# Kernel optimization log

Hardware: AMD Instinct MI355X
Metric: run time of the kernel (lower is better)

Reference implementation:

```python
import jax, jax.numpy as jnp
import numpy as np

B_, L_, STATE_DIM = 16, 1024, 17
D_MODEL, D_STATE, D_CONV, EXPAND, N_LAYERS = 512, 128, 4, 2, 6
HEADDIM = 64
D_INNER = EXPAND * D_MODEL              # 1024
NHEADS = D_INNER // HEADDIM             # 16
CONV_DIM = D_INNER + 2 * D_STATE        # 1280
D_IN_PROJ = 2 * D_INNER + 2 * D_STATE + NHEADS  # 2320


def _silu(x):
    return x * jax.nn.sigmoid(x)


def _layernorm(x, g, b, eps=1e-5):
    mu = jnp.mean(x, -1, keepdims=True)
    xc = x - mu
    var = jnp.mean(xc * xc, -1, keepdims=True)
    return xc * jax.lax.rsqrt(var + eps) * g + b


def _rope(x):
    # pairs are consecutive elements, matching x.view(B,L,d//2,2) in torch
    B, L, d = x.shape
    inv_freq = 1.0 / (10000.0 ** (jnp.arange(0, d, 2, dtype=jnp.float32) / d))
    freqs = jnp.arange(L, dtype=jnp.float32)[:, None] * inv_freq[None, :]  # [L, d/2]
    cos, sin = jnp.cos(freqs), jnp.sin(freqs)
    xr = x.reshape(B, L, d // 2, 2)
    x1, x2 = xr[..., 0], xr[..., 1]
    out = jnp.stack([x1 * cos - x2 * sin, x1 * sin + x2 * cos], axis=-1)
    return out.reshape(B, L, d)


def _causal_conv1d(x, w, b):
    # depthwise causal conv: x [B,L,C], w [C,K], b [C]
    K = w.shape[1]
    L = x.shape[1]
    xp = jnp.pad(x, ((0, 0), (K - 1, 0), (0, 0)))
    y = b
    for k in range(K):
        y = y + xp[:, k:k + L, :] * w[:, k]
    return y


def _mamba2(x, in_w, conv_w, conv_b, dt_bias, A_log, Dp, rms_w, out_w):
    # Mamba2 block (ngroups=1, headdim=64, gated RMSNorm, no proj biases)
    B, L, _ = x.shape
    zxbcdt = x @ in_w                              # [B,L,D_IN_PROJ]
    z = zxbcdt[..., :D_INNER]
    xBC = zxbcdt[..., D_INNER:D_INNER + CONV_DIM]
    dt = zxbcdt[..., D_INNER + CONV_DIM:]          # [B,L,H]
    xBC = _silu(_causal_conv1d(xBC, conv_w, conv_b))
    xs = xBC[..., :D_INNER].reshape(B, L, NHEADS, HEADDIM)
    Bm = xBC[..., D_INNER:D_INNER + D_STATE]       # [B,L,N]
    Cm = xBC[..., D_INNER + D_STATE:]              # [B,L,N]
    dt = jax.nn.softplus(dt + dt_bias)             # [B,L,H]
    A = -jnp.exp(A_log)                            # [H]
    decay = jnp.exp(dt * A)                        # [B,L,H]

    def step(h, inp):
        xt, Bt, Ct, dc, dtt = inp                  # [B,H,P],[B,N],[B,N],[B,H],[B,H]
        h = h * dc[..., None, None] + (dtt[..., None] * xt)[..., None] * Bt[:, None, None, :]
        yt = jnp.einsum('bhpn,bn->bhp', h, Ct)
        return h, yt

    h0 = jnp.zeros((B, NHEADS, HEADDIM, D_STATE), x.dtype)
    xs_t = jnp.moveaxis(xs, 1, 0)
    _, ys = jax.lax.scan(step, h0, (xs_t, jnp.moveaxis(Bm, 1, 0), jnp.moveaxis(Cm, 1, 0), jnp.moveaxis(decay, 1, 0), jnp.moveaxis(dt, 1, 0)))
    y = jnp.moveaxis(ys, 0, 1) + Dp[None, None, :, None] * xs  # [B,L,H,P]
    y = y.reshape(B, L, D_INNER)
    y = y * _silu(z)                               # gated
    y = y * jax.lax.rsqrt(jnp.mean(y * y, -1, keepdims=True) + 1e-5) * rms_w
    return y @ out_w


def setup_inputs():
    key = jax.random.key(0)
    ks = jax.random.split(key, 8)

    def rn(k, shape, scale):
        return jax.random.normal(k, shape, jnp.float32) * scale

    return dict(
        states=rn(ks[0], (B_, L_, STATE_DIM), 1.0),
        input_proj_w=rn(ks[1], (STATE_DIM, D_MODEL), STATE_DIM ** -0.5),
        input_proj_b=jnp.zeros((D_MODEL,), jnp.float32),
        ln_g=jnp.ones((N_LAYERS, D_MODEL), jnp.float32),
        ln_b=jnp.zeros((N_LAYERS, D_MODEL), jnp.float32),
        in_proj_w=rn(ks[2], (N_LAYERS, D_MODEL, D_IN_PROJ), D_MODEL ** -0.5),
        conv_w=rn(ks[3], (N_LAYERS, CONV_DIM, D_CONV), D_CONV ** -0.5),
        conv_b=jnp.zeros((N_LAYERS, CONV_DIM), jnp.float32),
        dt_bias=rn(ks[4], (N_LAYERS, NHEADS), 0.5) - 4.0,
        A_log=jnp.log(jax.random.uniform(ks[5], (N_LAYERS, NHEADS), jnp.float32, 1.0, 16.0)),
        D_param=jnp.ones((N_LAYERS, NHEADS), jnp.float32),
        rms_w=jnp.ones((N_LAYERS, D_INNER), jnp.float32),
        out_proj_w=rn(ks[6], (N_LAYERS, D_INNER, D_MODEL), D_INNER ** -0.5),
        post_ln_g=jnp.ones((D_MODEL,), jnp.float32),
        post_ln_b=jnp.zeros((D_MODEL,), jnp.float32),
        output_proj_w=rn(ks[7], (D_MODEL, D_MODEL), D_MODEL ** -0.5),
        output_proj_b=jnp.zeros((D_MODEL,), jnp.float32),
    )


def reference(states, input_proj_w, input_proj_b, ln_g, ln_b, in_proj_w, conv_w, conv_b,
              dt_bias, A_log, D_param, rms_w, out_proj_w, post_ln_g, post_ln_b,
              output_proj_w, output_proj_b):
    x = states @ input_proj_w + input_proj_b
    x = _rope(x)
    for l in range(N_LAYERS):
        h = _layernorm(x, ln_g[l], ln_b[l])
        h = _mamba2(h, in_proj_w[l], conv_w[l], conv_b[l], dt_bias[l], A_log[l],
                    D_param[l], rms_w[l], out_proj_w[l])
        x = x + h  # dropout is identity in eval mode
    x = _layernorm(x, post_ln_g, post_ln_b)
    return x @ output_proj_w + output_proj_b
```

## Files before the change

### kernel.cpp

```cpp
#include <hip/hip_runtime.h>
#include <hip/hip_bf16.h>
#include <cstdint>
#include <cstddef>


#define B_      16
#define L_      1024
#define NTOK    (B_ * L_)
#define DMODEL  512
#define DINNER  1024
#define NHEADS  16
#define HEADDIM 64
#define DSTATE  128
#define CONVDIM 1280
#define DINPROJ 2320
#define NPADT   2432
#define NLAYERS 6
#define LC      128
#define NC      8
#define SP      136
#define CCH     64
#define LOG2E   1.4426950408889634f

typedef short s8v  __attribute__((ext_vector_type(8)));
typedef float f4v  __attribute__((ext_vector_type(4)));
typedef unsigned short u8v __attribute__((ext_vector_type(8)));

__device__ __forceinline__ float b2f(unsigned short u) {
  unsigned v = ((unsigned)u) << 16;
  return __builtin_bit_cast(float, v);
}
__device__ __forceinline__ unsigned short f2b(float f) {
  unsigned u = __builtin_bit_cast(unsigned, f);
  u += 0x7fffu + ((u >> 16) & 1u);
  return (unsigned short)(u >> 16);
}
__device__ __forceinline__ void gl_lds16(const unsigned short* g, unsigned short* l) {
  __builtin_amdgcn_global_load_lds(
      (const __attribute__((address_space(1))) unsigned int*)g,
      (__attribute__((address_space(3))) unsigned int*)l, 16, 0, 0);
}

__global__ void k_flag(const unsigned int* __restrict__ lng_raw, int* __restrict__ flag) {
  *flag = (lng_raw[0] == 0x3F800000u) ? 0 : 1;
}

struct Cvt12 {
  const void* src[12];
  unsigned short* dst[12];
  int n[12];
};

__global__ __launch_bounds__(256) void k_convert_multi(
    Cvt12 jobs, const int* __restrict__ flag)
{
  const int f = *flag;
  const int e = blockIdx.y;
  const int n = jobs.n[e];
  const void* __restrict__ src = jobs.src[e];
  unsigned short* __restrict__ dst = jobs.dst[e];
  for (int i = blockIdx.x * 256 + threadIdx.x; i < n; i += gridDim.x * 256)
    dst[i] = f ? ((const unsigned short*)src)[i] : f2b(((const float*)src)[i]);
}

__global__ __launch_bounds__(96) void k_convertf3(
    const void* __restrict__ s0, const void* __restrict__ s1,
    const void* __restrict__ s2, float* __restrict__ dst,
    const int* __restrict__ flag)
{
  const int f = *flag;
  const int t = threadIdx.x;
  dst[t]       = f ? b2f(((const unsigned short*)s0)[t]) : ((const float*)s0)[t];
  dst[96 + t]  = f ? b2f(((const unsigned short*)s1)[t]) : ((const float*)s1)[t];
  dst[192 + t] = f ? b2f(((const unsigned short*)s2)[t]) : ((const float*)s2)[t];
}

__global__ __launch_bounds__(256) void k_transpose(
    const void* __restrict__ src, unsigned short* __restrict__ dst,
    const int K, const int Nsrc, const int Ndst, const int* __restrict__ flag)
{
  __shared__ unsigned short tile[32][33];
  const int f  = *flag;
  const int ko = blockIdx.x * 32, no = blockIdx.y * 32, z = blockIdx.z;
  const size_t soff = (size_t)z * K * Nsrc;
  const size_t doff = (size_t)z * Ndst * K;
  const int tx = threadIdx.x, ty = threadIdx.y;
  #pragma unroll
  for (int r = 0; r < 4; r++) {
    const int k = ko + ty + r * 8, n = no + tx;
    unsigned short v = 0;
    if (n < Nsrc)
      v = f ? ((const unsigned short*)src)[soff + (size_t)k * Nsrc + n]
            : f2b(((const float*)src)[soff + (size_t)k * Nsrc + n]);
    tile[ty + r * 8][tx] = v;
  }
  __syncthreads();
  #pragma unroll
  for (int r = 0; r < 4; r++) {
    const int n = no + ty + r * 8, k = ko + tx;
    dst[doff + (size_t)n * K + k] = tile[tx][ty + r * 8];
  }
}

__global__ __launch_bounds__(256) void k_inproj_rope(
    const unsigned short* __restrict__ states,
    const unsigned short* __restrict__ W,
    const unsigned short* __restrict__ bias,
    float* __restrict__ X)
{
  const int tok = blockIdx.x;
  const int t   = threadIdx.x;
  __shared__ float s[17];
  if (t < 17) s[t] = b2f(states[tok * 17 + t]);
  __syncthreads();
  const int d0 = 2 * t, d1 = d0 + 1;
  float x1 = b2f(bias[d0]);
  float x2 = b2f(bias[d1]);
  #pragma unroll
  for (int k = 0; k < 17; k++) {
    float sv = s[k];
    x1 = fmaf(sv, b2f(W[k * DMODEL + d0]), x1);
    x2 = fmaf(sv, b2f(W[k * DMODEL + d1]), x2);
  }
  const int l = tok & (L_ - 1);
  float invf = expf(-((float)d0 / (float)DMODEL) * 9.2103403719761836f);
  float fr = (float)l * invf;
  float sn, c;
  sincosf(fr, &sn, &c);
  X[(size_t)tok * DMODEL + d0] = x1 * c - x2 * sn;
  X[(size_t)tok * DMODEL + d1] = x1 * sn + x2 * c;
}

template<bool DTP>
__global__ __launch_bounds__(256) void k_layernorm_f(
    const float* __restrict__ X,
    const unsigned short* __restrict__ g,
    const unsigned short* __restrict__ b,
    unsigned short* __restrict__ out,
    const unsigned short* __restrict__ Wt,
    const float* __restrict__ dtb,
    const float* __restrict__ alog,
    float* __restrict__ DT, float* __restrict__ DEC)
{
  const int tok = blockIdx.x * 4 + (threadIdx.x >> 6);
  const int t   = threadIdx.x & 63;
  const float* row = X + (size_t)tok * DMODEL;
  float4 v0 = *(const float4*)(row + t * 4);
  float4 v1 = *(const float4*)(row + 256 + t * 4);
  float s  = v0.x + v0.y + v0.z + v0.w + v1.x + v1.y + v1.z + v1.w;
  float sq = v0.x*v0.x + v0.y*v0.y + v0.z*v0.z + v0.w*v0.w
           + v1.x*v1.x + v1.y*v1.y + v1.z*v1.z + v1.w*v1.w;
  #pragma unroll
  for (int m = 1; m < 64; m <<= 1) { s += __shfl_xor(s, m); sq += __shfl_xor(sq, m); }
  const float mu  = s  * (1.f / DMODEL);
  const float var = sq * (1.f / DMODEL) - mu * mu;
  const float rs  = rsqrtf(var + 1e-5f);
  const int c0 = t * 4, c1 = 256 + t * 4;
  float xn[8];
  xn[0] = (v0.x - mu) * rs * b2f(g[c0+0]) + b2f(b[c0+0]);
  xn[1] = (v0.y - mu) * rs * b2f(g[c0+1]) + b2f(b[c0+1]);
  xn[2] = (v0.z - mu) * rs * b2f(g[c0+2]) + b2f(b[c0+2]);
  xn[3] = (v0.w - mu) * rs * b2f(g[c0+3]) + b2f(b[c0+3]);
  xn[4] = (v1.x - mu) * rs * b2f(g[c1+0]) + b2f(b[c1+0]);
  xn[5] = (v1.y - mu) * rs * b2f(g[c1+1]) + b2f(b[c1+1]);
  xn[6] = (v1.z - mu) * rs * b2f(g[c1+2]) + b2f(b[c1+2]);
  xn[7] = (v1.w - mu) * rs * b2f(g[c1+3]) + b2f(b[c1+3]);
  {
    ushort4 o;
    o.x = f2b(xn[0]); o.y = f2b(xn[1]); o.z = f2b(xn[2]); o.w = f2b(xn[3]);
    *(ushort4*)(out + (size_t)tok * DMODEL + c0) = o;
    o.x = f2b(xn[4]); o.y = f2b(xn[5]); o.z = f2b(xn[6]); o.w = f2b(xn[7]);
    *(ushort4*)(out + (size_t)tok * DMODEL + c1) = o;
  }
  if constexpr (DTP) {
    float acc[16];
    #pragma unroll
    for (int hc = 0; hc < 16; hc++) {
      const unsigned short* wr = Wt + (size_t)(2304 + hc) * DMODEL;
      ushort4 wa = *(const ushort4*)(wr + c0);
      ushort4 wb = *(const ushort4*)(wr + c1);
      float a = 0.f;
      a = fmaf(xn[0], b2f(wa.x), a);
      a = fmaf(xn[1], b2f(wa.y), a);
      a = fmaf(xn[2], b2f(wa.z), a);
      a = fmaf(xn[3], b2f(wa.w), a);
      a = fmaf(xn[4], b2f(wb.x), a);
      a = fmaf(xn[5], b2f(wb.y), a);
      a = fmaf(xn[6], b2f(wb.z), a);
      a = fmaf(xn[7], b2f(wb.w), a);
      acc[hc] = a;
    }
    #pragma unroll
    for (int m = 1; m < 64; m <<= 1) {
      #pragma unroll
      for (int hc = 0; hc < 16; hc++) acc[hc] += __shfl_xor(acc[hc], m);
    }
    if (t < 16) {
      float x = acc[t] + dtb[t];
      float dt = (x > 20.f) ? x : log1pf(expf(x));
      float A = -expf(alog[t]);
      DT[(size_t)tok * NHEADS + t]  = dt;
      DEC[(size_t)tok * NHEADS + t] = expf(dt * A);
    }
  }
}

template<int MODE>
__global__ __launch_bounds__(256) void k_gemm_t(
    const unsigned short* __restrict__ A,
    const unsigned short* __restrict__ Wt,
    const int M, const int N, const int K,
    unsigned short* __restrict__ outb,
    float* __restrict__ resid,
    const unsigned short* __restrict__ bias,
    const int* __restrict__ flag)
{
  __shared__ __align__(16) unsigned short a_sh[128 * 64];
  __shared__ __align__(16) unsigned short b_sh[128 * 64];
  const int t    = threadIdx.x;
  const int wv   = t >> 6, lane = t & 63;
  const int l16  = lane & 15, quad = lane >> 4;
  const int gx   = gridDim.x;
  const int nwg  = gx * gridDim.y;
  const int bid  = blockIdx.y * gx + blockIdx.x;
  const int wgid = (bid & 7) * (nwg >> 3) + (bid >> 3);
  const int m0   = (wgid / gx) * 128;
  const int n0   = (wgid % gx) * 128;
  const int wr   = wv >> 1, wc = wv & 1;
  const int swz  = (l16 & 7) << 3;
  f4v acc[4][4] = {};
  for (int k0 = 0; k0 < K; k0 += 64) {
    #pragma unroll
    for (int i = 0; i < 4; i++) {
      const int cc  = (wv * 4 + i) * 64 + lane;
      const int row = cc >> 3;
      const int k8  = ((cc & 7) ^ (row & 7)) << 3;
      gl_lds16(A  + (size_t)(m0 + row) * K + k0 + k8, a_sh + cc * 8);
      gl_lds16(Wt + (size_t)(n0 + row) * K + k0 + k8, b_sh + cc * 8);
    }
    __syncthreads();
    #pragma unroll
    for (int kk = 0; kk < 2; kk++) {
      const int cs = (kk * 32 + quad * 8) ^ swz;
      s8v af[4], bf[4];
      #pragma unroll
      for (int mt = 0; mt < 4; mt++)
        af[mt] = *(const s8v*)(a_sh + (wr * 64 + mt * 16 + l16) * 64 + cs);
      #pragma unroll
      for (int nt = 0; nt < 4; nt++)
        bf[nt] = *(const s8v*)(b_sh + (wc * 64 + nt * 16 + l16) * 64 + cs);
      #pragma unroll
      for (int mt = 0; mt < 4; mt++)
        #pragma unroll
        for (int nt = 0; nt < 4; nt++)
          acc[mt][nt] = __builtin_amdgcn_mfma_f32_16x16x32_bf16(af[mt], bf[nt], acc[mt][nt], 0, 0, 0);
    }
    __syncthreads();
  }
  const int fv = (MODE == 2) ? *flag : 0;
  #pragma unroll
  for (int mt = 0; mt < 4; mt++) {
    #pragma unroll
    for (int nt = 0; nt < 4; nt++) {
      #pragma unroll
      for (int r = 0; r < 4; r++) {
        const int m = m0 + wr * 64 + mt * 16 + quad * 4 + r;
        const int n = n0 + wc * 64 + nt * 16 + l16;
        float v = acc[mt][nt][r];
        if (MODE == 0) {
          if (n < 2304) outb[(size_t)m * DINPROJ + n] = f2b(v);
        } else if (MODE == 1) {
          resid[(size_t)m * N + n] += v;
        } else {
          v += b2f(bias[n]);
          if (fv) outb[(size_t)m * N + n] = f2b(v);
          else    ((float*)resid)[(size_t)m * N + n] = v;
        }
      }
    }
  }
}

__global__ __launch_bounds__(256) void k_conv(
    const unsigned short* __restrict__ zx,
    const unsigned short* __restrict__ cw,
    const unsigned short* __restrict__ cb,
    unsigned short* __restrict__ out)
{
  const int c  = blockIdx.x * 256 + threadIdx.x;
  const int bc = blockIdx.y;
  const int b  = bc >> 4, ch = bc & 15;
  const int l0 = ch * CCH;
  const int tok0 = b * L_ + l0;
  const float w0 = b2f(cw[c * 4 + 0]), w1 = b2f(cw[c * 4 + 1]);
  const float w2 = b2f(cw[c * 4 + 2]), w3 = b2f(cw[c * 4 + 3]);
  const float bias = b2f(cb[c]);
  const unsigned short* src = zx + (size_t)tok0 * DINPROJ + DINNER + c;
  float x0 = 0.f, x1 = 0.f, x2 = 0.f;
  if (l0 > 0) {
    x0 = b2f(src[-3 * DINPROJ]);
    x1 = b2f(src[-2 * DINPROJ]);
    x2 = b2f(src[-1 * DINPROJ]);
  }
  unsigned short* dst = out + (size_t)tok0 * CONVDIM + c;
  for (int s = 0; s < CCH; s++) {
    const float x3 = b2f(src[(size_t)s * DINPROJ]);
    float a = bias;
    a = fmaf(x0, w0, a);
    a = fmaf(x1, w1, a);
    a = fmaf(x2, w2, a);
    a = fmaf(x3, w3, a);
    dst[(size_t)s * CONVDIM] = f2b(a / (1.f + expf(-a)));
    x0 = x1; x1 = x2; x2 = x3;
  }
}

__global__ __launch_bounds__(256) void k_scan(
    const unsigned short* __restrict__ xbc,
    const float* __restrict__ DT,
    const float* __restrict__ DEC,
    const float* __restrict__ Dp,
    unsigned short* __restrict__ yout)
{
  const int bh = blockIdx.x;
  const int b  = bh >> 4, h = bh & 15;
  const int t  = threadIdx.x;
  __shared__ __align__(16) float sxbc[320];
  __shared__ float ssc[2];
  const int ngrp = t & 15, pgrp = t >> 4;
  const int n0 = ngrp * 8, p0 = pgrp * 4;
  float hs[4][8] = {};
  const float Dh = Dp[h];
  for (int ts = 0; ts < L_; ts++) {
    const int tok = (b << 10) + ts;
    if (t < 40) {
      const int j = t * 8;
      const int col = (j < 64) ? (h * HEADDIM + j) : (960 + j);
      u8v v = *(const u8v*)(xbc + (size_t)tok * CONVDIM + col);
      float* d = &sxbc[j];
      #pragma unroll
      for (int q = 0; q < 8; q++) d[q] = b2f(v[q]);
    }
    if (t == 63) {
      ssc[0] = DT[(size_t)tok * NHEADS + h];
      ssc[1] = DEC[(size_t)tok * NHEADS + h];
    }
    __syncthreads();
    float xa[4]; *(float4*)xa = *(const float4*)&sxbc[p0];
    float Bv[8], Cv[8];
    #pragma unroll
    for (int q = 0; q < 8; q++) { Bv[q] = sxbc[64 + n0 + q]; Cv[q] = sxbc[192 + n0 + q]; }
    const float dts = ssc[0], dec = ssc[1];
    float yp[4];
    #pragma unroll
    for (int p = 0; p < 4; p++) {
      const float dtx = dts * xa[p];
      float a = 0.f;
      #pragma unroll
      for (int n = 0; n < 8; n++) {
        hs[p][n] = fmaf(hs[p][n], dec, dtx * Bv[n]);
        a = fmaf(hs[p][n], Cv[n], a);
      }
      yp[p] = a;
    }
    #pragma unroll
    for (int m = 1; m < 16; m <<= 1) {
      #pragma unroll
      for (int p = 0; p < 4; p++) yp[p] += __shfl_xor(yp[p], m);
    }
    if (ngrp == 0) {
      ushort4 o;
      o.x = f2b(yp[0] + Dh * xa[0]);
      o.y = f2b(yp[1] + Dh * xa[1]);
      o.z = f2b(yp[2] + Dh * xa[2]);
      o.w = f2b(yp[3] + Dh * xa[3]);
      *(ushort4*)(yout + (size_t)tok * DINPROJ + DINNER + h * HEADDIM + p0) = o;
    }
    __syncthreads();
  }
}

__global__ __launch_bounds__(512) void k_scan_chunk_mfma(
    const unsigned short* __restrict__ xbc,
    const float* __restrict__ DT,
    const float* __restrict__ alog,
    const float* __restrict__ Dp,
    unsigned short* __restrict__ yout,
    unsigned short* __restrict__ SLOC,
    float* __restrict__ PP)
{
  const int c  = blockIdx.x;
  const int bh = blockIdx.y;
  const int b  = bh >> 4, h = bh & 15;
  const int t  = threadIdx.x;
  const int wv = t >> 6, lane = t & 63;
  const int l16 = lane & 15, quad = lane >> 4;
  const int tok0 = (b << 10) + c * LC;

  __shared__ __align__(16) short sBig[128][SP];
  __shared__ __align__(16) short sXt[64][SP];
  __shared__ float sLc[128], sdt[128], sw3[128];

  if (wv == 0) {
    float d0 = DT[(size_t)(tok0 + lane) * NHEADS + h];
    float d1 = DT[(size_t)(tok0 + 64 + lane) * NHEADS + h];
    float v = d0;
    #pragma unroll
    for (int off = 1; off < 64; off <<= 1) {
      float u = __shfl_up(v, off);
      if (lane >= off) v += u;
    }
    float tot = __shfl(v, 63);
    float w = d1;
    #pragma unroll
    for (int off = 1; off < 64; off <<= 1) {
      float u = __shfl_up(w, off);
      if (lane >= off) w += u;
    }
    w += tot;
    const float A2 = -expf(alog[h]) * LOG2E;
    const float lo0 = A2 * v, lo1 = A2 * w;
    sdt[lane] = d0;  sdt[64 + lane] = d1;
    sLc[lane] = lo0; sLc[64 + lane] = lo1;
    const float L127 = __shfl(lo1, 63);
    sw3[lane]      = d0 * exp2f(L127 - lo0);
    sw3[64 + lane] = d1 * exp2f(L127 - lo1);
    float* pp = PP + (size_t)(bh * NC + c) * LC;
    pp[lane]      = exp2f(lo0);
    pp[64 + lane] = exp2f(lo1);
  }
  {
    const int s0   = (t & 63) * 2;
    const int part = t >> 6;
    const unsigned short* r0 = xbc + (size_t)(tok0 + s0) * CONVDIM;
    const unsigned short* r1 = r0 + CONVDIM;
    u8v xa = *(const u8v*)(r0 + h * 64 + part * 8);
    u8v xb = *(const u8v*)(r1 + h * 64 + part * 8);
    #pragma unroll
    for (int j = 0; j < 8; j++)
      *(unsigned*)&sXt[part * 8 + j][s0] = ((unsigned)xa[j]) | (((unsigned)xb[j]) << 16);
    #pragma unroll
    for (int q = 0; q < 2; q++) {
      u8v b0 = *(const u8v*)(r0 + 1024 + part * 16 + q * 8);
      u8v b1 = *(const u8v*)(r1 + 1024 + part * 16 + q * 8);
      #pragma unroll
      for (int j = 0; j < 8; j++)
        *(unsigned*)&sBig[part * 16 + q * 8 + j][s0] =
            ((unsigned)b0[j]) | (((unsigned)b1[j]) << 16);
    }
  }
  __syncthreads();

  {
    unsigned short* dst = SLOC + (((size_t)(bh * NC + c)) << 13);
    const int ncol = wv * 16 + l16;
    f4v acc[4] = {};
    #pragma unroll
    for (int kk = 0; kk < 4; kk++) {
      s8v bb = *(const s8v*)&sBig[ncol][kk * 32 + quad * 8];
      float4 w0 = *(const float4*)&sw3[kk * 32 + quad * 8];
      float4 w1 = *(const float4*)&sw3[kk * 32 + quad * 8 + 4];
      s8v bw;
      bw[0] = (short)f2b(b2f((unsigned short)bb[0]) * w0.x);
      bw[1] = (short)f2b(b2f((unsigned short)bb[1]) * w0.y);
      bw[2] = (short)f2b(b2f((unsigned short)bb[2]) * w0.z);
      bw[3] = (short)f2b(b2f((unsigned short)bb[3]) * w0.w);
      bw[4] = (short)f2b(b2f((unsigned short)bb[4]) * w1.x);
      bw[5] = (short)f2b(b2f((unsigned short)bb[5]) * w1.y);
      bw[6] = (short)f2b(b2f((unsigned short)bb[6]) * w1.z);
      bw[7] = (short)f2b(b2f((unsigned short)bb[7]) * w1.w);
      __builtin_amdgcn_s_setprio(1);
      #pragma unroll
      for (int pt = 0; pt < 4; pt++) {
        s8v ax = *(const s8v*)&sXt[pt * 16 + l16][kk * 32 + quad * 8];
        acc[pt] = __builtin_amdgcn_mfma_f32_16x16x32_bf16(ax, bw, acc[pt], 0, 0, 0);
      }
      __builtin_amdgcn_s_setprio(0);
    }
    #pragma unroll
    for (int pt = 0; pt < 4; pt++)
      #pragma unroll
      for (int r = 0; r < 4; r++)
        dst[(pt * 16 + quad * 4 + r) * DSTATE + ncol] = f2b(acc[pt][r]);
  }

  {
    const float Dh = Dp[h];
    const int tt = wv;
    const int trow = tok0 + tt * 16 + l16;
    s8v af[4];
    #pragma unroll
    for (int kk = 0; kk < 4; kk++)
      af[kk] = *(const s8v*)(xbc + (size_t)trow * CONVDIM + 1152 + kk * 32 + quad * 8);
    const float ref = sLc[tt * 16];
    float et[4];
    #pragma unroll
    for (int r = 0; r < 4; r++)
      et[r] = exp2f(sLc[tt * 16 + quad * 4 + r] - ref);
    s8v bfn[4];
    #pragma unroll
    for (int kk = 0; kk < 4; kk++)
      bfn[kk] = *(const s8v*)(xbc + (size_t)(tok0 + l16) * CONVDIM + 1024 + kk * 32 + quad * 8);
    for (int st = 0; st <= tt; st++) {
      s8v bfc[4];
      #pragma unroll
      for (int kk = 0; kk < 4; kk++) bfc[kk] = bfn[kk];
      if (st < tt) {
        const int srow = tok0 + (st + 1) * 16 + l16;
        #pragma unroll
        for (int kk = 0; kk < 4; kk++)
          bfn[kk] = *(const s8v*)(xbc + (size_t)srow * CONVDIM + 1024 + kk * 32 + quad * 8);
      }
      f4v acc = {};
      __builtin_amdgcn_s_setprio(1);
      #pragma unroll
      for (int kk = 0; kk < 4; kk++)
        acc = __builtin_amdgcn_mfma_f32_16x16x32_bf16(af[kk], bfc[kk], acc, 0, 0, 0);
      __builtin_amdgcn_s_setprio(0);
      const int scol = st * 16 + l16;
      const float Ls = sLc[scol], dts = sdt[scol];
      if (st < tt) {
        const float fs = exp2f(ref - Ls) * dts;
        #pragma unroll
        for (int r = 0; r < 4; r++)
          sBig[tt * 16 + quad * 4 + r][scol] = (short)f2b(acc[r] * (et[r] * fs));
      } else {
        #pragma unroll
        for (int r = 0; r < 4; r++) {
          const int trw = tt * 16 + quad * 4 + r;
          const float mv = (scol <= trw) ? exp2f(sLc[trw] - Ls) * dts : 0.f;
          sBig[trw][scol] = (short)f2b(acc[r] * mv);
        }
      }
    }
    if ((tt & 1) == 0) {
      #pragma unroll
      for (int r = 0; r < 4; r++)
        sBig[tt * 16 + quad * 4 + r][(tt + 1) * 16 + l16] = 0;
    }
    const int nk = tt / 2 + 1;
    const int tcol = tt * 16 + l16;
    f4v accy[4] = {};
    for (int kk = 0; kk < nk; kk++) {
      s8v bf = *(const s8v*)&sBig[tcol][kk * 32 + quad * 8];
      __builtin_amdgcn_s_setprio(1);
      #pragma unroll
      for (int pt = 0; pt < 4; pt++) {
        s8v ax = *(const s8v*)&sXt[pt * 16 + l16][kk * 32 + quad * 8];
        accy[pt] = __builtin_amdgcn_mfma_f32_16x16x32_bf16(ax, bf, accy[pt], 0, 0, 0);
      }
      __builtin_amdgcn_s_setprio(0);
    }
    const int tok = tok0 + tcol;
    unsigned short* yrow = yout + (size_t)tok * DINPROJ + DINNER + h * 64;
    #pragma unroll
    for (int pt = 0; pt < 4; pt++) {
      ushort4 o;
      unsigned short* oa = (unsigned short*)&o;
      #pragma unroll
      for (int r = 0; r < 4; r++) {
        const int p = pt * 16 + quad * 4 + r;
        oa[r] = f2b(accy[pt][r] + Dh * b2f((unsigned short)sXt[p][tcol]));
      }
      *(ushort4*)(yrow + pt * 16 + quad * 4) = o;
    }
  }
}

__global__ __launch_bounds__(256) void k_scan_prop(
    unsigned short* __restrict__ SLOC,
    const float* __restrict__ PP)
{
  const int bh = blockIdx.x;
  const int t  = threadIdx.x;
  float hst[32];
  #pragma unroll
  for (int j = 0; j < 32; j++) hst[j] = 0.f;
  for (int c = 0; c < NC - 1; c++) {
    const size_t slot = ((size_t)(bh * NC + c)) << 13;
    const float Dc = PP[(size_t)(bh * NC + c) * LC + (LC - 1)];
    unsigned short* base = SLOC + slot + t * 32;
    u8v v[4];
    #pragma unroll
    for (int j = 0; j < 4; j++) v[j] = *(const u8v*)(base + j * 8);
    #pragma unroll
    for (int j = 0; j < 32; j++)
      hst[j] = fmaf(hst[j], Dc, b2f(v[j >> 3][j & 7]));
    #pragma unroll
    for (int j = 0; j < 4; j++) {
      u8v o;
      #pragma unroll
      for (int q = 0; q < 8; q++) o[q] = f2b(hst[j * 8 + q]);
      *(u8v*)(base + j * 8) = o;
    }
  }
}

__global__ __launch_bounds__(256) void k_scan_ystate(
    const unsigned short* __restrict__ xbc,
    const unsigned short* __restrict__ SLOC,
    const float* __restrict__ PP,
    unsigned short* __restrict__ yout)
{
  const int c  = blockIdx.x + 1;
  const int bh = blockIdx.y;
  const int b  = bh >> 4, h = bh & 15;
  const int t  = threadIdx.x;
  const int wv = t >> 6, lane = t & 63;
  const int l16 = lane & 15, quad = lane >> 4;
  __shared__ float sp[LC];
  if (t < LC) sp[t] = PP[(size_t)(bh * NC + c) * LC + t];
  __syncthreads();
  const int tok0 = (b << 10) + c * LC;
  const unsigned short* hsrc = SLOC + (((size_t)(bh * NC + c - 1)) << 13);
  f4v acc[2][4] = {};
  for (int k0 = 0; k0 < DSTATE; k0 += 32) {
    s8v af[2], bf[4];
    #pragma unroll
    for (int i = 0; i < 2; i++) {
      const int m = wv * 32 + i * 16 + l16;
      af[i] = *(const s8v*)(xbc + (size_t)(tok0 + m) * CONVDIM + 1152 + k0 + quad * 8);
    }
    #pragma unroll
    for (int nt = 0; nt < 4; nt++)
      bf[nt] = *(const s8v*)(hsrc + (nt * 16 + l16) * DSTATE + k0 + quad * 8);
    #pragma unroll
    for (int i = 0; i < 2; i++)
      #pragma unroll
      for (int nt = 0; nt < 4; nt++)
        acc[i][nt] = __builtin_amdgcn_mfma_f32_16x16x32_bf16(af[i], bf[nt], acc[i][nt], 0, 0, 0);
  }
  #pragma unroll
  for (int i = 0; i < 2; i++) {
    #pragma unroll
    for (int nt = 0; nt < 4; nt++) {
      #pragma unroll
      for (int r = 0; r < 4; r++) {
        const int m = wv * 32 + i * 16 + quad * 4 + r;
        const int p = nt * 16 + l16;
        unsigned short* yp = yout + (size_t)(tok0 + m) * DINPROJ + DINNER + h * HEADDIM + p;
        *yp = f2b(b2f(*yp) + sp[m] * acc[i][nt][r]);
      }
    }
  }
}

__global__ __launch_bounds__(256) void k_gate_rms(
    const unsigned short* __restrict__ buf1,
    const unsigned short* __restrict__ rmsw,
    unsigned short* __restrict__ out)
{
  const int tok = blockIdx.x * 4 + (threadIdx.x >> 6);
  const int t   = threadIdx.x & 63;
  const unsigned short* zrow = buf1 + (size_t)tok * DINPROJ;
  const unsigned short* yrow = zrow + DINNER;
  float gv[16];
  float sq = 0.f;
  #pragma unroll
  for (int q = 0; q < 4; q++) {
    const int c = q * 256 + t * 4;
    ushort4 z4 = *(const ushort4*)(zrow + c);
    ushort4 y4 = *(const ushort4*)(yrow + c);
    const unsigned short* za = (const unsigned short*)&z4;
    const unsigned short* ya = (const unsigned short*)&y4;
    #pragma unroll
    for (int j = 0; j < 4; j++) {
      float z = b2f(za[j]), y = b2f(ya[j]);
      float g = y * (z / (1.f + expf(-z)));
      gv[q * 4 + j] = g;
      sq = fmaf(g, g, sq);
    }
  }
  #pragma unroll
  for (int m = 1; m < 64; m <<= 1) sq += __shfl_xor(sq, m);
  const float rs = rsqrtf(sq * (1.f / DINNER) + 1e-5f);
  #pragma unroll
  for (int q = 0; q < 4; q++) {
    const int c = q * 256 + t * 4;
    ushort4 o;
    unsigned short* oa = (unsigned short*)&o;
    #pragma unroll
    for (int j = 0; j < 4; j++) oa[j] = f2b(gv[q * 4 + j] * rs * b2f(rmsw[c + j]));
    *(ushort4*)(out + (size_t)tok * DINNER + c) = o;
  }
}

extern "C" void kernel_launch(void* const* d_in, const int* in_sizes, int n_in,
                              void* d_out, int out_size, void* d_ws, size_t ws_size,
                              hipStream_t stream)
{
  (void)in_sizes; (void)n_in; (void)out_size;

  char* ws = (char*)d_ws;
  float*          X       = (float*)(ws);
  unsigned short* BUF1    = (unsigned short*)(ws + 33554432);
  unsigned short* BUF2    = (unsigned short*)(ws + 109576192);
  float*          DT      = (float*)(ws + 151519232);
  float*          DEC     = (float*)(ws + 152567808);
  unsigned short* CWINT   = (unsigned short*)(ws + 153616384);
  unsigned short* CWOUTT  = (unsigned short*)(ws + 168558592);
  unsigned short* CWFINT  = (unsigned short*)(ws + 174850048);
  unsigned short* CIPW    = (unsigned short*)(ws + 175374336);
  unsigned short* CSTATES = (unsigned short*)(ws + 175391744);
  unsigned short* CSMALL  = (unsigned short*)(ws + 175948800);
  float*          CF32    = (float*)(ws + 176054272);
  int*            FLAG    = (int*)(ws + 176055424);
  unsigned short* SLOC    = (unsigned short*)(ws + 176055552);
  float*          PP      = (float*)(ws + 209609984);
  const bool usechunk = (ws_size >= 210658560ull);
  unsigned short* HN = BUF2;

  unsigned short* Cipb   = CSMALL + 0;
  unsigned short* Clng   = CSMALL + 512;
  unsigned short* Clnb   = CSMALL + 3584;
  unsigned short* Cconvw = CSMALL + 6656;
  unsigned short* Cconvb = CSMALL + 37376;
  unsigned short* Crmsw  = CSMALL + 45056;
  unsigned short* Cpostg = CSMALL + 51200;
  unsigned short* Cpostb = CSMALL + 51712;
  unsigned short* Cfinb  = CSMALL + 52224;
  float* Cdtb  = CF32 + 0;
  float* Calog = CF32 + 96;
  float* Cdpar = CF32 + 192;

  k_flag<<<1, 1, 0, stream>>>((const unsigned int*)d_in[3], FLAG);

  Cvt12 jobs;
  jobs.src[0]  = d_in[0];  jobs.dst[0]  = CSTATES; jobs.n[0]  = NTOK * 17;
  jobs.src[1]  = d_in[1];  jobs.dst[1]  = CIPW;    jobs.n[1]  = 17 * DMODEL;
  jobs.src[2]  = d_in[2];  jobs.dst[2]  = Cipb;    jobs.n[2]  = DMODEL;
  jobs.src[3]  = d_in[3];  jobs.dst[3]  = Clng;    jobs.n[3]  = NLAYERS * DMODEL;
  jobs.src[4]  = d_in[4];  jobs.dst[4]  = Clnb;    jobs.n[4]  = NLAYERS * DMODEL;
  jobs.src[5]  = d_in[6];  jobs.dst[5]  = Cconvw;  jobs.n[5]  = NLAYERS * CONVDIM * 4;
  jobs.src[6]  = d_in[7];  jobs.dst[6]  = Cconvb;  jobs.n[6]  = NLAYERS * CONVDIM;
  jobs.src[7]  = d_in[11]; jobs.dst[7]  = Crmsw;   jobs.n[7]  = NLAYERS * DINNER;
  jobs.src[8]  = d_in[13]; jobs.dst[8]  = Cpostg;  jobs.n[8]  = DMODEL;
  jobs.src[9]  = d_in[14]; jobs.dst[9]  = Cpostb;  jobs.n[9]  = DMODEL;
  jobs.src[10] = d_in[16]; jobs.dst[10] = Cfinb;   jobs.n[10] = DMODEL;
  jobs.src[11] = d_in[0];  jobs.dst[11] = CSTATES; jobs.n[11] = 0;
  k_convert_multi<<<dim3(64, 11), 256, 0, stream>>>(jobs, FLAG);
  k_convertf3<<<1, 96, 0, stream>>>(d_in[8], d_in[9], d_in[10], CF32, FLAG);

  k_transpose<<<dim3(16, 76, 6), dim3(32, 8), 0, stream>>>(
      d_in[5], CWINT, DMODEL, DINPROJ, NPADT, FLAG);
  k_transpose<<<dim3(32, 16, 6), dim3(32, 8), 0, stream>>>(
      d_in[12], CWOUTT, DINNER, DMODEL, DMODEL, FLAG);
  k_transpose<<<dim3(16, 16, 1), dim3(32, 8), 0, stream>>>(
      d_in[15], CWFINT, DMODEL, DMODEL, DMODEL, FLAG);

  k_inproj_rope<<<NTOK, 256, 0, stream>>>(CSTATES, CIPW, Cipb, X);

  for (int l = 0; l < NLAYERS; l++) {
    k_layernorm_f<true><<<NTOK / 4, 256, 0, stream>>>(
        X, Clng + l * DMODEL, Clnb + l * DMODEL, HN,
        CWINT + (size_t)l * NPADT * DMODEL,
        Cdtb + l * NHEADS, Calog + l * NHEADS, DT, DEC);
    k_gemm_t<0><<<dim3(NPADT / 128, NTOK / 128), 256, 0, stream>>>(
        HN, CWINT + (size_t)l * NPADT * DMODEL, NTOK, NPADT, DMODEL,
        BUF1, nullptr, nullptr, FLAG);
    k_conv<<<dim3(CONVDIM / 256, B_ * (L_ / CCH)), 256, 0, stream>>>(
        BUF1, Cconvw + l * CONVDIM * 4, Cconvb + l * CONVDIM, BUF2);
    if (usechunk) {
      k_scan_chunk_mfma<<<dim3(NC, 256), 512, 0, stream>>>(
          BUF2, DT, Calog + l * NHEADS, Cdpar + l * NHEADS, BUF1, SLOC, PP);
      k_scan_prop<<<256, 256, 0, stream>>>(SLOC, PP);
      k_scan_ystate<<<dim3(NC - 1, 256), 256, 0, stream>>>(BUF2, SLOC, PP, BUF1);
    } else {
      k_scan<<<256, 256, 0, stream>>>(BUF2, DT, DEC, Cdpar + l * NHEADS, BUF1);
    }
    k_gate_rms<<<NTOK / 4, 256, 0, stream>>>(BUF1, Crmsw + l * DINNER, HN);
    k_gemm_t<1><<<dim3(DMODEL / 128, NTOK / 128), 256, 0, stream>>>(
        HN, CWOUTT + (size_t)l * DMODEL * DINNER, NTOK, DMODEL, DINNER,
        nullptr, X, nullptr, FLAG);
  }

  k_layernorm_f<false><<<NTOK / 4, 256, 0, stream>>>(
      X, Cpostg, Cpostb, HN, nullptr, nullptr, nullptr, nullptr, nullptr);
  k_gemm_t<2><<<dim3(DMODEL / 128, NTOK / 128), 256, 0, stream>>>(
      HN, CWFINT, NTOK, DMODEL, DMODEL,
      (unsigned short*)d_out, (float*)d_out, Cfinb, FLAG);
}
```

Before: 1.913 ms.

## Fuse inter-chunk state propagation into ystate kernel, dropping prop launch

Removes the separate sequential state-propagation kernel. Each ystate block now recomputes the prefix-propagated state for its chunk from the per-chunk local states, stages it in shared memory as bf16, and feeds the MFMA B operand from LDS. This saves one launch per layer and the write-back of propagated states. In exchange it adds redundant work that grows with the chunk index (up to 7 reads per block). It also changes rounding slightly, because the accumulation now stays in fp32 across chunks instead of being rounded to bf16 after each chunk.

New measurement: 1.838 ms (median of 2 runs). 3.9% less time.

```diff
diff --git a/kernel.cpp b/kernel.cpp
--- a/kernel.cpp
+++ b/kernel.cpp
@@ -567,35 +567,6 @@
   }
 }
 
-__global__ __launch_bounds__(256) void k_scan_prop(
-    unsigned short* __restrict__ SLOC,
-    const float* __restrict__ PP)
-{
-  const int bh = blockIdx.x;
-  const int t  = threadIdx.x;
-  float hst[32];
-  #pragma unroll
-  for (int j = 0; j < 32; j++) hst[j] = 0.f;
-  for (int c = 0; c < NC - 1; c++) {
-    const size_t slot = ((size_t)(bh * NC + c)) << 13;
-    const float Dc = PP[(size_t)(bh * NC + c) * LC + (LC - 1)];
-    unsigned short* base = SLOC + slot + t * 32;
-    u8v v[4];
-    #pragma unroll
-    for (int j = 0; j < 4; j++) v[j] = *(const u8v*)(base + j * 8);
-    #pragma unroll
-    for (int j = 0; j < 32; j++)
-      hst[j] = fmaf(hst[j], Dc, b2f(v[j >> 3][j & 7]));
-    #pragma unroll
-    for (int j = 0; j < 4; j++) {
-      u8v o;
-      #pragma unroll
-      for (int q = 0; q < 8; q++) o[q] = f2b(hst[j * 8 + q]);
-      *(u8v*)(base + j * 8) = o;
-    }
-  }
-}
-
 __global__ __launch_bounds__(256) void k_scan_ystate(
     const unsigned short* __restrict__ xbc,
     const unsigned short* __restrict__ SLOC,
@@ -609,10 +580,36 @@
   const int wv = t >> 6, lane = t & 63;
   const int l16 = lane & 15, quad = lane >> 4;
   __shared__ float sp[LC];
+  __shared__ __align__(16) unsigned short hs[64 * SP];
   if (t < LC) sp[t] = PP[(size_t)(bh * NC + c) * LC + t];
+  {
+    float hst[32];
+    #pragma unroll
+    for (int q = 0; q < 32; q++) hst[q] = 0.f;
+    for (int j = 0; j < c; j++) {
+      const size_t slot = ((size_t)(bh * NC + j)) << 13;
+      const float Dc = PP[(size_t)(bh * NC + j) * LC + (LC - 1)];
+      const unsigned short* base = SLOC + slot + t * 32;
+      u8v v[4];
+      #pragma unroll
+      for (int q = 0; q < 4; q++) v[q] = *(const u8v*)(base + q * 8);
+      #pragma unroll
+      for (int q = 0; q < 32; q++)
+        hst[q] = fmaf(hst[q], Dc, b2f(v[q >> 3][q & 7]));
+    }
+    const int p  = t >> 2;
+    const int n0 = (t & 3) * 32;
+    unsigned short* dst = hs + p * SP + n0;
+    #pragma unroll
+    for (int q = 0; q < 4; q++) {
+      u8v o;
+      #pragma unroll
+      for (int j = 0; j < 8; j++) o[j] = f2b(hst[q * 8 + j]);
+      *(u8v*)(dst + q * 8) = o;
+    }
+  }
   __syncthreads();
   const int tok0 = (b << 10) + c * LC;
-  const unsigned short* hsrc = SLOC + (((size_t)(bh * NC + c - 1)) << 13);
   f4v acc[2][4] = {};
   for (int k0 = 0; k0 < DSTATE; k0 += 32) {
     s8v af[2], bf[4];
@@ -623,7 +620,7 @@
     }
     #pragma unroll
     for (int nt = 0; nt < 4; nt++)
-      bf[nt] = *(const s8v*)(hsrc + (nt * 16 + l16) * DSTATE + k0 + quad * 8);
+      bf[nt] = *(const s8v*)(hs + (nt * 16 + l16) * SP + k0 + quad * 8);
     #pragma unroll
     for (int i = 0; i < 2; i++)
       #pragma unroll
@@ -763,7 +760,6 @@
     if (usechunk) {
       k_scan_chunk_mfma<<<dim3(NC, 256), 512, 0, stream>>>(
           BUF2, DT, Calog + l * NHEADS, Cdpar + l * NHEADS, BUF1, SLOC, PP);
-      k_scan_prop<<<256, 256, 0, stream>>>(SLOC, PP);
       k_scan_ystate<<<dim3(NC - 1, 256), 256, 0, stream>>>(BUF2, SLOC, PP, BUF1);
     } else {
       k_scan<<<256, 256, 0, stream>>>(BUF2, DT, DEC, Cdpar + l * NHEADS, BUF1);
```
